# Kernel tuning notes

Measured on AMD Instinct MI355X. Metric: run time of the kernel, lower is better.

The kernel has to match this reference:

```python
import jax, jax.numpy as jnp
import numpy as np

N_NODES = 100000


def _gcn_layer(x, W, b, src, dst, norm_edge, self_norm):
    # GCNConv: out = D^{-1/2}(A+I)D^{-1/2} X W + b
    h = x @ W                                   # [N, out]
    msgs = h[src] * norm_edge[:, None]          # [E, out] gather + scale
    out = jax.ops.segment_sum(msgs, dst, num_segments=N_NODES)
    out = out + self_norm[:, None] * h          # self-loop contribution
    return out + b


def _norms(edge_index):
    src, dst = edge_index[0], edge_index[1]
    # degree includes the self-loop weight of 1 (PyG gcn_norm)
    deg = jax.ops.segment_sum(jnp.ones(src.shape[0], jnp.float32), dst,
                              num_segments=N_NODES) + 1.0
    deg_isqrt = jnp.where(deg > 0, jax.lax.rsqrt(deg), 0.0)
    norm_edge = deg_isqrt[src] * deg_isqrt[dst]  # per-edge norm
    self_norm = deg_isqrt * deg_isqrt            # norm for i->i self loop
    return src, dst, norm_edge, self_norm


def setup_inputs() -> dict:
    key = jax.random.key(0)
    ks = jax.random.split(key, 10)
    channels = [128, 64, 32]
    dims = list(zip(channels[:-1], channels[1:])) + \
           list(zip(channels[::-1][:-1], channels[::-1][1:]))  # enc + dec
    inp = {
        "x": jax.random.normal(ks[0], (N_NODES, 128), jnp.float32),
        "edge_index": jax.random.randint(ks[1], (2, 1600000), 0, N_NODES,
                                         dtype=jnp.int64),
    }
    for i, (din, dout) in enumerate(dims):
        scale = 1.0 / np.sqrt(din)
        inp[f"W{i+1}"] = jax.random.normal(ks[2 + 2 * i], (din, dout),
                                           jnp.float32) * scale
        inp[f"b{i+1}"] = jnp.zeros((dout,), jnp.float32)
    return inp


def reference(x, edge_index, W1, b1, W2, b2, W3, b3, W4, b4):
    src, dst, norm_edge, self_norm = _norms(edge_index)
    # Dropout is identity in eval mode; ReLU follows every GCNConv
    for W, b in ((W1, b1), (W2, b2), (W3, b3), (W4, b4)):
        x = jax.nn.relu(_gcn_layer(x, W, b, src, dst, norm_edge, self_norm))
    return x
```

## Files before the change

kernel.cpp:

```cpp
#include <hip/hip_runtime.h>
#include <hip/hip_fp16.h>


#define DEV static __device__ __forceinline__
#define ELL_CAP 48
#define BSHIFT 8
#define BRANGE 256
#define BCAP 5120
#define EPT 16
#define TILE (256 * EPT)
#define MAXNB 1024
#define SPILL_CAP 65536

typedef _Float16 f16x8 __attribute__((ext_vector_type(8)));
typedef float f32x4 __attribute__((ext_vector_type(4)));

DEV int eidx(const void* ei, long long i, int is64) {
  if (is64) return (int)((const long long*)ei)[i];
  return ((const int*)ei)[i];
}

__global__ void prep_kernel(const int* __restrict__ w, long long nwords,
                            int* __restrict__ flag, int* __restrict__ bmeta,
                            int nmeta) {
  __shared__ int nz;
  if (threadIdx.x == 0) nz = 0;
  __syncthreads();
  for (int i = threadIdx.x; i < nmeta; i += blockDim.x) bmeta[i] = 0;
  long long samples = nwords / 2;
  if (samples > 4096) samples = 4096;
  for (long long i = threadIdx.x; i < samples; i += blockDim.x) {
    if (w[2 * i + 1] != 0) atomicOr(&nz, 1);
  }
  __syncthreads();
  if (threadIdx.x == 0) *flag = (nz == 0) ? 1 : 0;
}

DEV void scatter_body(char* smem, const void* __restrict__ ei,
                      const int* __restrict__ flagp, long long E,
                      int* __restrict__ bcnt, unsigned int* __restrict__ bdata,
                      int* __restrict__ spill_cnt, int2* __restrict__ spill,
                      int nb, int bx) {
  int* lcnt = (int*)smem;
  int* gbase = lcnt + MAXNB;
  const int tid = threadIdx.x;
  const long long base = (long long)bx * TILE;
  for (int i = tid; i < nb; i += 256) lcnt[i] = 0;
  __syncthreads();
  const int is64 = *flagp;
  unsigned upack[EPT];
  int ub[EPT];
#pragma unroll
  for (int i = 0; i < EPT; i++) {
    const long long e = base + i * 256 + tid;
    ub[i] = -1;
    if (e < E) {
      const int s = eidx(ei, e, is64);
      const int d = eidx(ei, E + e, is64);
      const int b = d >> BSHIFT;
      ub[i] = b;
      upack[i] = ((unsigned)s << BSHIFT) | (unsigned)(d & (BRANGE - 1));
      atomicAdd(&lcnt[b], 1);
    }
  }
  __syncthreads();
  for (int i = tid; i < nb; i += 256) {
    const int c = lcnt[i];
    gbase[i] = (c > 0) ? atomicAdd(&bcnt[i], c) : 0;
    lcnt[i] = 0;
  }
  __syncthreads();
#pragma unroll
  for (int i = 0; i < EPT; i++) {
    if (ub[i] >= 0) {
      const int b = ub[i];
      const int slot = atomicAdd(&lcnt[b], 1);
      const int pos = gbase[b] + slot;
      if (pos < BCAP) {
        bdata[(long long)b * BCAP + pos] = upack[i];
      } else {
        const int sp = atomicAdd(spill_cnt, 1);
        if (sp < SPILL_CAP)
          spill[sp] = make_int2((int)(upack[i] >> BSHIFT),
                                (b << BSHIFT) | (int)(upack[i] & (BRANGE - 1)));
      }
    }
  }
}

template <int DIN, int DOUT, int EPI, bool A16, bool OUTH>
DEV void gemm_body(char* smem, const void* __restrict__ Av,
                   const float* __restrict__ W, const float* __restrict__ bias,
                   const float* __restrict__ dis, void* __restrict__ outv,
                   int n, int bx) {
  constexpr int NCB = DOUT / 16;
  constexpr int NT = DIN / 32;
  constexpr int ROWS = 64;
  _Float16* sB = (_Float16*)smem;
  const int tid = threadIdx.x;
  for (int idx = tid; idx < NT * NCB * 64; idx += 256) {
    const int l = idx & 63;
    const int cb = (idx >> 6) % NCB;
    const int t = idx / (64 * NCB);
    const int c = cb * 16 + (l & 15);
    const int k0 = t * 32 + ((l >> 4) << 3);
    _Float16* dst = &sB[idx * 8];
#pragma unroll
    for (int j = 0; j < 8; j++) dst[j] = (_Float16)W[(k0 + j) * DOUT + c];
  }
  __syncthreads();
  const int wv = tid >> 6;
  const int lane = tid & 63;
  const int lrow = lane & 15;
  const int lk = (lane >> 4) << 3;
  const int row0 = bx * ROWS;
  const int agr = row0 + wv * 16 + lrow;
  const bool inb = agr < n;
  f16x8 afr[NT];
#pragma unroll
  for (int t = 0; t < NT; t++) {
    if (A16) {
      const __half* A = (const __half*)Av;
      uint4 v = make_uint4(0u, 0u, 0u, 0u);
      if (inb) v = *(const uint4*)&A[(long long)agr * DIN + t * 32 + lk];
      union { uint4 u; f16x8 h; } cv;
      cv.u = v;
      afr[t] = cv.h;
    } else {
      const float* A = (const float*)Av;
      float4 v0 = make_float4(0.f, 0.f, 0.f, 0.f);
      float4 v1 = v0;
      if (inb) {
        v0 = *(const float4*)&A[(long long)agr * DIN + t * 32 + lk];
        v1 = *(const float4*)&A[(long long)agr * DIN + t * 32 + lk + 4];
      }
      f16x8 h;
      h[0] = (_Float16)v0.x; h[1] = (_Float16)v0.y;
      h[2] = (_Float16)v0.z; h[3] = (_Float16)v0.w;
      h[4] = (_Float16)v1.x; h[5] = (_Float16)v1.y;
      h[6] = (_Float16)v1.z; h[7] = (_Float16)v1.w;
      afr[t] = h;
    }
  }
  f32x4 acc[NCB];
#pragma unroll
  for (int cb = 0; cb < NCB; cb++) acc[cb] = (f32x4){0.f, 0.f, 0.f, 0.f};
#pragma unroll
  for (int t = 0; t < NT; t++) {
#pragma unroll
    for (int cb = 0; cb < NCB; cb++) {
      const f16x8 b = *(const f16x8*)&sB[((t * NCB + cb) * 64 + lane) * 8];
      acc[cb] = __builtin_amdgcn_mfma_f32_16x16x32_f16(afr[t], b, acc[cb], 0, 0, 0);
    }
  }
  const int crow0 = row0 + wv * 16 + ((lane >> 4) << 2);
  const int ccol = lane & 15;
#pragma unroll
  for (int cb = 0; cb < NCB; cb++) {
    const int col = cb * 16 + ccol;
#pragma unroll
    for (int i = 0; i < 4; i++) {
      const int gr = crow0 + i;
      if (gr < n) {
        float v = acc[cb][i];
        if (EPI == 0) {
          v *= dis[gr];
        } else if (EPI >= 1) {
          v = fmaxf(v + bias[col], 0.f);
          if (EPI == 2) v *= dis[gr];
        }
        if (OUTH)
          ((__half*)outv)[(long long)gr * DOUT + col] = __float2half(v);
        else
          ((float*)outv)[(long long)gr * DOUT + col] = v;
      }
    }
  }
}

template <int DIN, int DOUT, int EPI, bool A16, bool OUTH>
__global__ __launch_bounds__(256) void gemm_mfma(
    const void* __restrict__ Av, const float* __restrict__ W,
    const float* __restrict__ bias, const float* __restrict__ dis,
    void* __restrict__ outv, int n) {
  constexpr int SM = (DIN / 32) * (DOUT / 16) * 64 * 8 * 2;
  __shared__ __align__(16) char smem[SM];
  gemm_body<DIN, DOUT, EPI, A16, OUTH>(smem, Av, W, bias, dis, outv, n,
                                       blockIdx.x);
}

__global__ __launch_bounds__(256) void fused_scatter_gemm(
    const void* __restrict__ Av, const float* __restrict__ W,
    void* __restrict__ outv, int n, int ntiles,
    const void* __restrict__ ei, const int* __restrict__ flagp, long long E,
    int* __restrict__ bcnt, unsigned int* __restrict__ bdata,
    int* __restrict__ spill_cnt, int2* __restrict__ spill, int nb) {
  __shared__ __align__(16) char smem[16384];
  if ((int)blockIdx.x < ntiles) {
    scatter_body(smem, ei, flagp, E, bcnt, bdata, spill_cnt, spill, nb,
                 blockIdx.x);
  } else {
    gemm_body<128, 64, -1, false, true>(smem, Av, W, nullptr, nullptr, outv, n,
                                        blockIdx.x - ntiles);
  }
}

__global__ __launch_bounds__(256) void ell_build(
    const int* __restrict__ bcnt, const unsigned int* __restrict__ bdata,
    int* __restrict__ cursor, int* __restrict__ ell, float* __restrict__ dis,
    int n) {
  const int b = blockIdx.x;
  const int lo = b << BSHIFT;
  const int npb = min(BRANGE, n - lo);
  __shared__ int scur[BRANGE];
  __shared__ int sell[BRANGE * ELL_CAP];
  for (int i = threadIdx.x; i < BRANGE; i += 256) scur[i] = 0;
  __syncthreads();
  const int cnt = min(bcnt[b], BCAP);
  const unsigned int* __restrict__ bd = bdata + (long long)b * BCAP;
  for (int i = threadIdx.x; i < cnt; i += 256) {
    const unsigned u = bd[i];
    const int ld = u & (BRANGE - 1);
    const int p = atomicAdd(&scur[ld], 1);
    if (p < ELL_CAP) sell[ld * ELL_CAP + p] = (int)(u >> BSHIFT);
  }
  __syncthreads();
  int4* __restrict__ e4 = (int4*)(ell + (long long)lo * ELL_CAP);
  const int4* __restrict__ s4 = (const int4*)sell;
  for (int i = threadIdx.x; i < npb * (ELL_CAP / 4); i += 256) e4[i] = s4[i];
  for (int i = threadIdx.x; i < npb; i += 256) {
    cursor[lo + i] = scur[i];
    dis[lo + i] = rsqrtf((float)scur[i] + 1.0f);
  }
}

__global__ void spill_fix(const int* __restrict__ spill_cnt,
                          const int2* __restrict__ spill,
                          int* __restrict__ cursor, int* __restrict__ ell,
                          float* __restrict__ dis) {
  const int m = min(*spill_cnt, SPILL_CAP);
  const int stride = gridDim.x * blockDim.x;
  for (int i = blockIdx.x * blockDim.x + threadIdx.x; i < m; i += stride) {
    const int2 e = spill[i];
    const int pos = atomicAdd(&cursor[e.y], 1);
    if (pos < ELL_CAP) ell[(long long)e.y * ELL_CAP + pos] = e.x;
    const float cand = rsqrtf((float)(pos + 1) + 1.0f);
    atomicMin((unsigned int*)&dis[e.y], __float_as_uint(cand));
  }
}

DEV void acc8(float* a, const uint4& v) {
  union { uint4 u; __half2 h[4]; } cv;
  cv.u = v;
#pragma unroll
  for (int j = 0; j < 4; j++) {
    const float2 f = __half22float2(cv.h[j]);
    a[2 * j] += f.x;
    a[2 * j + 1] += f.y;
  }
}

template <int D, int EPI, bool OUT16>
__global__ __launch_bounds__(256) void aggregate(
    const int* __restrict__ cursor, const int* __restrict__ ell,
    const __half* __restrict__ g, const float* __restrict__ dis,
    const float* __restrict__ bias, void* __restrict__ outv, int n) {
  constexpr int TPN = D / 8;
  constexpr int NPB = 256 / TPN;
  const int node = blockIdx.x * NPB + threadIdx.x / TPN;
  const int c = (threadIdx.x & (TPN - 1)) * 8;
  if (node >= n) return;
  int deg = cursor[node];
  if (deg > ELL_CAP) deg = ELL_CAP;
  const int* __restrict__ row = ell + (long long)node * ELL_CAP;
  float a0[8], a1[8], a2[8], a3[8];
  {
    union { uint4 u; __half2 h[4]; } cv;
    cv.u = *(const uint4*)&g[(long long)node * D + c];
#pragma unroll
    for (int j = 0; j < 4; j++) {
      const float2 f = __half22float2(cv.h[j]);
      a0[2 * j] = f.x;
      a0[2 * j + 1] = f.y;
    }
#pragma unroll
    for (int j = 0; j < 8; j++) { a1[j] = 0.f; a2[j] = 0.f; a3[j] = 0.f; }
  }
  int p = 0;
  for (; p + 7 < deg; p += 8) {
    const int s0 = row[p + 0];
    const int s1 = row[p + 1];
    const int s2 = row[p + 2];
    const int s3 = row[p + 3];
    const int s4 = row[p + 4];
    const int s5 = row[p + 5];
    const int s6 = row[p + 6];
    const int s7 = row[p + 7];
    const uint4 v0 = *(const uint4*)&g[(long long)s0 * D + c];
    const uint4 v1 = *(const uint4*)&g[(long long)s1 * D + c];
    const uint4 v2 = *(const uint4*)&g[(long long)s2 * D + c];
    const uint4 v3 = *(const uint4*)&g[(long long)s3 * D + c];
    const uint4 v4 = *(const uint4*)&g[(long long)s4 * D + c];
    const uint4 v5 = *(const uint4*)&g[(long long)s5 * D + c];
    const uint4 v6 = *(const uint4*)&g[(long long)s6 * D + c];
    const uint4 v7 = *(const uint4*)&g[(long long)s7 * D + c];
    acc8(a0, v0); acc8(a1, v1); acc8(a2, v2); acc8(a3, v3);
    acc8(a0, v4); acc8(a1, v5); acc8(a2, v6); acc8(a3, v7);
  }
  for (; p < deg; ++p) {
    const uint4 v = *(const uint4*)&g[(long long)row[p] * D + c];
    acc8(a0, v);
  }
  float s[8];
#pragma unroll
  for (int j = 0; j < 8; j++) s[j] = (a0[j] + a1[j]) + (a2[j] + a3[j]);
  const float dn = dis[node];
  if (EPI == 0) {
#pragma unroll
    for (int j = 0; j < 8; j++) s[j] *= dn;
  } else {
#pragma unroll
    for (int j = 0; j < 8; j++) s[j] = fmaxf(dn * s[j] + bias[c + j], 0.f);
    if (EPI == 2) {
#pragma unroll
      for (int j = 0; j < 8; j++) s[j] *= dn;
    }
  }
  if (OUT16) {
    __half* oh = (__half*)outv;
    union { uint4 u; __half2 h[4]; } pk;
#pragma unroll
    for (int j = 0; j < 4; j++)
      pk.h[j] = __floats2half2_rn(s[2 * j], s[2 * j + 1]);
    *(uint4*)&oh[(long long)node * D + c] = pk.u;
  } else {
    float* op = (float*)outv;
    *(float4*)&op[(long long)node * D + c] = make_float4(s[0], s[1], s[2], s[3]);
    *(float4*)&op[(long long)node * D + c + 4] =
        make_float4(s[4], s[5], s[6], s[7]);
  }
}

__global__ __launch_bounds__(256) void aggregate1_raw(
    const int* __restrict__ cursor, const int* __restrict__ ell,
    const __half* __restrict__ g, const float* __restrict__ dis,
    const float* __restrict__ bias, void* __restrict__ outv, int n) {
  constexpr int D = 64;
  constexpr int TPN = D / 8;
  constexpr int NPB = 256 / TPN;
  const int node = blockIdx.x * NPB + threadIdx.x / TPN;
  const int c = (threadIdx.x & (TPN - 1)) * 8;
  if (node >= n) return;
  int deg = cursor[node];
  if (deg > ELL_CAP) deg = ELL_CAP;
  const int* __restrict__ row = ell + (long long)node * ELL_CAP;
  const float dn = dis[node];
  float a0[8], a1[8];
  {
    union { uint4 u; __half2 h[4]; } cv;
    cv.u = *(const uint4*)&g[(long long)node * D + c];
#pragma unroll
    for (int j = 0; j < 4; j++) {
      const float2 f = __half22float2(cv.h[j]);
      a0[2 * j] = dn * f.x;
      a0[2 * j + 1] = dn * f.y;
    }
#pragma unroll
    for (int j = 0; j < 8; j++) a1[j] = 0.f;
  }
  int p = 0;
  for (; p + 1 < deg; p += 2) {
    const int s0 = row[p];
    const int s1 = row[p + 1];
    const float d0 = dis[s0];
    const float d1 = dis[s1];
    union { uint4 u; __half2 h[4]; } c0, c1;
    c0.u = *(const uint4*)&g[(long long)s0 * D + c];
    c1.u = *(const uint4*)&g[(long long)s1 * D + c];
#pragma unroll
    for (int j = 0; j < 4; j++) {
      const float2 f0 = __half22float2(c0.h[j]);
      const float2 f1 = __half22float2(c1.h[j]);
      a0[2 * j] += d0 * f0.x;
      a0[2 * j + 1] += d0 * f0.y;
      a1[2 * j] += d1 * f1.x;
      a1[2 * j + 1] += d1 * f1.y;
    }
  }
  for (; p < deg; ++p) {
    const int s0 = row[p];
    const float d0 = dis[s0];
    union { uint4 u; __half2 h[4]; } c0;
    c0.u = *(const uint4*)&g[(long long)s0 * D + c];
#pragma unroll
    for (int j = 0; j < 4; j++) {
      const float2 f0 = __half22float2(c0.h[j]);
      a0[2 * j] += d0 * f0.x;
      a0[2 * j + 1] += d0 * f0.y;
    }
  }
  float s[8];
#pragma unroll
  for (int j = 0; j < 8; j++)
    s[j] = fmaxf(dn * (a0[j] + a1[j]) + bias[c + j], 0.f);
  __half* oh = (__half*)outv;
  union { uint4 u; __half2 h[4]; } pk;
#pragma unroll
  for (int j = 0; j < 4; j++)
    pk.h[j] = __floats2half2_rn(s[2 * j], s[2 * j + 1]);
  *(uint4*)&oh[(long long)node * D + c] = pk.u;
}

extern "C" void kernel_launch(void* const* d_in, const int* in_sizes, int n_in,
                              void* d_out, int out_size, void* d_ws,
                              size_t ws_size, hipStream_t stream) {
  const float* x = (const float*)d_in[0];
  const void* ei = d_in[1];
  const float* W1 = (const float*)d_in[2];
  const float* b1 = (const float*)d_in[3];
  const float* W2 = (const float*)d_in[4];
  const float* b2 = (const float*)d_in[5];
  const float* W3 = (const float*)d_in[6];
  const float* b3 = (const float*)d_in[7];
  const float* W4 = (const float*)d_in[8];
  const float* b4 = (const float*)d_in[9];
  float* out = (float*)d_out;

  const long long E = (long long)in_sizes[1] / 2;
  const int N = in_sizes[0] / 128;
  const int NB = (N + BRANGE - 1) / BRANGE;
  const int NTILES = (int)((E + TILE - 1) / TILE);

  char* ws = (char*)d_ws;
  auto align256 = [](size_t o) { return (o + 255) & ~(size_t)255; };
  size_t off = 0;
  int* flag = (int*)(ws + off);      off = align256(off + 16);
  int* cursor = (int*)(ws + off);    off = align256(off + (size_t)N * 4);
  float* dis = (float*)(ws + off);   off = align256(off + (size_t)N * 4);
  int* bmeta = (int*)(ws + off);     off = align256(off + ((size_t)NB + 16) * 4);
  int2* spill = (int2*)(ws + off);   off = align256(off + (size_t)SPILL_CAP * 8);
  unsigned int* bdata = (unsigned int*)(ws + off);
  off = align256(off + (size_t)NB * BCAP * 4);
  int* ell = (int*)(ws + off);       off = align256(off + (size_t)N * ELL_CAP * 4);
  __half* gh1 = (__half*)(ws + off); off = align256(off + (size_t)N * 64 * 2);
  __half* gh2 = (__half*)(ws + off); off = align256(off + (size_t)N * 32 * 2);
  __half* gh3 = (__half*)(ws + off); off = align256(off + (size_t)N * 32 * 2);
  __half* gh4 = (__half*)(ws + off); off = align256(off + (size_t)N * 64 * 2);
  __half* oh1 = (__half*)(ws + off); off = align256(off + (size_t)N * 64 * 2);
  __half* zh3 = (__half*)(ws + off); off = align256(off + (size_t)N * 32 * 2);
  __half* zh4 = (__half*)(ws + off); off = align256(off + (size_t)N * 64 * 2);
  int* bcnt = bmeta;
  int* spill_cnt = bmeta + NB;
  (void)ws_size; (void)n_in; (void)out_size;

  const int GB = (N + 63) / 64;

  prep_kernel<<<1, 256, 0, stream>>>((const int*)ei, 2 * E, flag, bmeta,
                                     NB + 16);
  fused_scatter_gemm<<<NTILES + GB, 256, 0, stream>>>(
      x, W1, gh1, N, NTILES, ei, flag, E, bcnt, bdata, spill_cnt, spill, NB);
  ell_build<<<NB, 256, 0, stream>>>(bcnt, bdata, cursor, ell, dis, N);
  spill_fix<<<64, 256, 0, stream>>>(spill_cnt, spill, cursor, ell, dis);

  aggregate1_raw<<<(N + 31) / 32, 256, 0, stream>>>(
      cursor, ell, gh1, dis, b1, oh1, N);
  gemm_mfma<64, 32, 0, true, true><<<GB, 256, 0, stream>>>(
      oh1, W2, nullptr, dis, gh2, N);
  aggregate<32, 2, true><<<(N + 63) / 64, 256, 0, stream>>>(
      cursor, ell, gh2, dis, b2, gh3, N);
  aggregate<32, 0, true><<<(N + 63) / 64, 256, 0, stream>>>(
      cursor, ell, gh3, dis, nullptr, zh3, N);
  gemm_mfma<32, 64, 2, true, true><<<GB, 256, 0, stream>>>(
      zh3, W3, b3, dis, gh4, N);
  aggregate<64, 0, true><<<(N + 31) / 32, 256, 0, stream>>>(
      cursor, ell, gh4, dis, nullptr, zh4, N);
  gemm_mfma<64, 128, 1, true, false><<<GB, 256, 0, stream>>>(
      zh4, W4, b4, dis, out, N);
}
```

Baseline: 212.4 us.

## Split fused scatter/GEMM kernel and use 1024-thread scatter blocks

```diff
diff --git a/kernel.cpp b/kernel.cpp
--- a/kernel.cpp
+++ b/kernel.cpp
@@ -7,8 +7,8 @@
 #define BSHIFT 8
 #define BRANGE 256
 #define BCAP 5120
-#define EPT 16
-#define TILE (256 * EPT)
+#define SEPT 4
+#define TILE (1024 * SEPT)
 #define MAXNB 1024
 #define SPILL_CAP 65536
 
@@ -36,23 +36,22 @@
   if (threadIdx.x == 0) *flag = (nz == 0) ? 1 : 0;
 }
 
-DEV void scatter_body(char* smem, const void* __restrict__ ei,
-                      const int* __restrict__ flagp, long long E,
-                      int* __restrict__ bcnt, unsigned int* __restrict__ bdata,
-                      int* __restrict__ spill_cnt, int2* __restrict__ spill,
-                      int nb, int bx) {
-  int* lcnt = (int*)smem;
-  int* gbase = lcnt + MAXNB;
+__global__ __launch_bounds__(1024) void scatter_kernel(
+    const void* __restrict__ ei, const int* __restrict__ flagp, long long E,
+    int* __restrict__ bcnt, unsigned int* __restrict__ bdata,
+    int* __restrict__ spill_cnt, int2* __restrict__ spill, int nb) {
+  __shared__ int lcnt[MAXNB];
+  __shared__ int gbase[MAXNB];
   const int tid = threadIdx.x;
-  const long long base = (long long)bx * TILE;
-  for (int i = tid; i < nb; i += 256) lcnt[i] = 0;
+  const long long base = (long long)blockIdx.x * TILE;
+  for (int i = tid; i < nb; i += 1024) lcnt[i] = 0;
   __syncthreads();
   const int is64 = *flagp;
-  unsigned upack[EPT];
-  int ub[EPT];
-#pragma unroll
-  for (int i = 0; i < EPT; i++) {
-    const long long e = base + i * 256 + tid;
+  unsigned upack[SEPT];
+  int ub[SEPT];
+#pragma unroll
+  for (int i = 0; i < SEPT; i++) {
+    const long long e = base + i * 1024 + tid;
     ub[i] = -1;
     if (e < E) {
       const int s = eidx(ei, e, is64);
@@ -64,14 +63,14 @@
     }
   }
   __syncthreads();
-  for (int i = tid; i < nb; i += 256) {
+  for (int i = tid; i < nb; i += 1024) {
     const int c = lcnt[i];
     gbase[i] = (c > 0) ? atomicAdd(&bcnt[i], c) : 0;
     lcnt[i] = 0;
   }
   __syncthreads();
 #pragma unroll
-  for (int i = 0; i < EPT; i++) {
+  for (int i = 0; i < SEPT; i++) {
     if (ub[i] >= 0) {
       const int b = ub[i];
       const int slot = atomicAdd(&lcnt[b], 1);
@@ -189,22 +188,6 @@
                                        blockIdx.x);
 }
 
-__global__ __launch_bounds__(256) void fused_scatter_gemm(
-    const void* __restrict__ Av, const float* __restrict__ W,
-    void* __restrict__ outv, int n, int ntiles,
-    const void* __restrict__ ei, const int* __restrict__ flagp, long long E,
-    int* __restrict__ bcnt, unsigned int* __restrict__ bdata,
-    int* __restrict__ spill_cnt, int2* __restrict__ spill, int nb) {
-  __shared__ __align__(16) char smem[16384];
-  if ((int)blockIdx.x < ntiles) {
-    scatter_body(smem, ei, flagp, E, bcnt, bdata, spill_cnt, spill, nb,
-                 blockIdx.x);
-  } else {
-    gemm_body<128, 64, -1, false, true>(smem, Av, W, nullptr, nullptr, outv, n,
-                                        blockIdx.x - ntiles);
-  }
-}
-
 __global__ __launch_bounds__(256) void ell_build(
     const int* __restrict__ bcnt, const unsigned int* __restrict__ bdata,
     int* __restrict__ cursor, int* __restrict__ ell, float* __restrict__ dis,
@@ -457,8 +440,10 @@
 
   prep_kernel<<<1, 256, 0, stream>>>((const int*)ei, 2 * E, flag, bmeta,
                                      NB + 16);
-  fused_scatter_gemm<<<NTILES + GB, 256, 0, stream>>>(
-      x, W1, gh1, N, NTILES, ei, flag, E, bcnt, bdata, spill_cnt, spill, NB);
+  scatter_kernel<<<NTILES, 1024, 0, stream>>>(ei, flag, E, bcnt, bdata,
+                                              spill_cnt, spill, NB);
+  gemm_mfma<128, 64, -1, false, true><<<GB, 256, 0, stream>>>(
+      x, W1, nullptr, nullptr, gh1, N);
   ell_build<<<NB, 256, 0, stream>>>(bcnt, bdata, cursor, ell, dis, N);
   spill_fix<<<64, 256, 0, stream>>>(spill_cnt, spill, cursor, ell, dis);
 
```

Result: slower. 218.4 us (+2.9%).
